# Kernel optimization log

Hardware: AMD Instinct MI355X
Metric: run time of the kernel (lower is better)

Reference implementation:

```python
import jax, jax.numpy as jnp
import numpy as np

# ---- Clifford algebra Cl(3,0) setup: blades ordered by grade ----
_BLADES = [(), (1,), (2,), (3,), (1, 2), (1, 3), (2, 3), (1, 2, 3)]
_SUBSPACES = np.array([1, 3, 3, 1])  # grade sizes
_GRADE_SLICES = [(0, 1), (1, 4), (4, 7), (7, 8)]


def _blade_mul(a, b):
    """Geometric product of two basis blades in Cl(3,0) (metric +1,+1,+1)."""
    arr = list(a) + list(b)
    sign = 1
    n = len(arr)
    for i in range(n):
        for j in range(n - 1):
            if arr[j] > arr[j + 1]:
                arr[j], arr[j + 1] = arr[j + 1], arr[j]
                sign = -sign
    res = []
    i = 0
    while i < len(arr):
        if i + 1 < len(arr) and arr[i] == arr[i + 1]:
            i += 2  # e_i * e_i = +1
        else:
            res.append(arr[i]); i += 1
    return sign, tuple(res)


def build_cayley():
    idx = {b: i for i, b in enumerate(_BLADES)}
    C = np.zeros((8, 8, 8), np.float32)
    for i, bi in enumerate(_BLADES):
        for k, bk in enumerate(_BLADES):
            s, r = _blade_mul(bi, bk)
            C[i, idx[r], k] = s
    return jnp.asarray(C)  # cayley[i, j, k]: coeff of blade j in (blade_i * blade_k)


def mv_linear(x, W):
    # x: (b, seq_in, 8); W: (seq_out, seq_in, 4) -> expand per-grade weight over blades
    Wfull = jnp.repeat(W, _SUBSPACES, axis=-1)  # (out, in, 8)
    return jnp.einsum('bmi,nmi->bni', x, Wfull)


def normalize(x, a):
    # x: (b, s, 8); a: (max_seq, 4)
    seq = x.shape[1]
    norms = jnp.concatenate(
        [jnp.linalg.norm(x[..., s:e], axis=-1, keepdims=True) for s, e in _GRADE_SLICES],
        axis=-1)  # (b, s, 4)
    s_a = jax.nn.sigmoid(a[:seq])                      # (s, 4)
    norms = s_a * (norms - 1.0) + 1.0                  # (b, s, 4)
    norms = jnp.repeat(norms, _SUBSPACES, axis=-1)     # (b, s, 8)
    return x / (norms + 1e-6)


def setup_inputs() -> dict:
    key = jax.random.key(0)
    k1, k2, k3 = jax.random.split(key, 3)
    B, S, D = 2, 2048, 8
    scale = 1.0 / np.sqrt(S)
    x = jax.random.normal(k1, (B, S, D), jnp.float32)
    Wq = jax.random.normal(k2, (S, S, 4), jnp.float32) * scale
    Wk = jax.random.normal(k3, (S, S, 4), jnp.float32) * scale
    a = jnp.zeros((3000, 4), jnp.float32)  # NormalizationLayer init=0
    return {"x": x, "Wq": Wq, "Wk": Wk, "a": a}


def reference(x, Wq, Wk, a):
    cayley = build_cayley()
    q = normalize(mv_linear(x, Wq), a)  # (b, s, 8)
    k = normalize(mv_linear(x, Wk), a)  # (b, s, 8)
    # pairwise geometric product: out[b,s,t,j] = sum_{i,k} q[b,s,i] cayley[i,j,k] k[b,t,k]
    tmp = jnp.einsum('bsi,ijk->bsjk', q, cayley)        # (b, s, 8, 8)
    out = jnp.einsum('bsjk,btk->bstj', tmp, k)          # (b, s, t, 8)
    return out
```

## Files before the change

### kernel.cpp

```cpp
#include <hip/hip_runtime.h>
#include <cmath>

#define SEQ 2048
#define BATCH 2

typedef float v4f __attribute__((ext_vector_type(4)));

__global__ __launch_bounds__(256) void qk_kernel(
    const float* __restrict__ x,
    const float* __restrict__ Wq,
    const float* __restrict__ Wk,
    const float* __restrict__ a,
    float* __restrict__ qout,
    float* __restrict__ kout)
{
    const int n   = blockIdx.x;
    const int tid = threadIdx.x;

    float acc[32];
#pragma unroll
    for (int v = 0; v < 32; v++) acc[v] = 0.f;

    const v4f* wq4 = (const v4f*)(Wq + (size_t)n * SEQ * 4);
    const v4f* wk4 = (const v4f*)(Wk + (size_t)n * SEQ * 4);
    const v4f* x4  = (const v4f*)x;

    for (int m = tid; m < SEQ; m += 256) {
        v4f wq = wq4[m];
        v4f wk = wk4[m];
        const float wqg[4] = {wq.x, wq.y, wq.z, wq.w};
        const float wkg[4] = {wk.x, wk.y, wk.z, wk.w};
#pragma unroll
        for (int b = 0; b < BATCH; b++) {
            v4f xa = x4[((size_t)b * SEQ + m) * 2];
            v4f xb = x4[((size_t)b * SEQ + m) * 2 + 1];
            const float xv[8] = {xa.x, xa.y, xa.z, xa.w, xb.x, xb.y, xb.z, xb.w};
            const int g[8] = {0, 1, 1, 1, 2, 2, 2, 3};
#pragma unroll
            for (int i = 0; i < 8; i++) {
                acc[0 * 16 + b * 8 + i] += wqg[g[i]] * xv[i];
                acc[1 * 16 + b * 8 + i] += wkg[g[i]] * xv[i];
            }
        }
    }

#pragma unroll
    for (int v = 0; v < 32; v++) {
#pragma unroll
        for (int off = 32; off >= 1; off >>= 1)
            acc[v] += __shfl_down(acc[v], off, 64);
    }

    __shared__ float red[4][32];
    __shared__ float fin[32];
    const int wave = tid >> 6;
    const int lane = tid & 63;
    if (lane == 0) {
#pragma unroll
        for (int v = 0; v < 32; v++) red[wave][v] = acc[v];
    }
    __syncthreads();
    if (tid < 32) fin[tid] = red[0][tid] + red[1][tid] + red[2][tid] + red[3][tid];
    __syncthreads();

    if (tid < 4) {
        const int t_sel = tid >> 1;
        const int b     = tid & 1;
        float v[8];
#pragma unroll
        for (int i = 0; i < 8; i++) v[i] = fin[t_sel * 16 + b * 8 + i];

        float nr[4];
        nr[0] = fabsf(v[0]);
        nr[1] = sqrtf(v[1] * v[1] + v[2] * v[2] + v[3] * v[3]);
        nr[2] = sqrtf(v[4] * v[4] + v[5] * v[5] + v[6] * v[6]);
        nr[3] = fabsf(v[7]);

        float sc[4];
#pragma unroll
        for (int gg = 0; gg < 4; gg++) {
            float sg = 1.f / (1.f + __expf(-a[n * 4 + gg]));
            sc[gg]   = 1.f / (sg * (nr[gg] - 1.f) + 1.f + 1e-6f);
        }

        float* dst = (t_sel ? kout : qout) + ((size_t)b * SEQ + n) * 8;
        const int g[8] = {0, 1, 1, 1, 2, 2, 2, 3};
#pragma unroll
        for (int i = 0; i < 8; i++) dst[i] = v[i] * sc[g[i]];
    }
}

__global__ __launch_bounds__(256) void gp_kernel(
    const float* __restrict__ q,
    const float* __restrict__ k,
    float* __restrict__ out)
{
    const int bs  = blockIdx.x;
    const int b   = bs >> 11;
    const int s   = bs & (SEQ - 1);
    const int tid = threadIdx.x;

    __shared__ float qs[8];
    if (tid < 8) qs[tid] = q[((size_t)b * SEQ + s) * 8 + tid];
    __syncthreads();
    const float q0 = qs[0], q1 = qs[1], q2 = qs[2], q3 = qs[3],
                q4 = qs[4], q5 = qs[5], q6 = qs[6], q7 = qs[7];

    const v4f* kp  = (const v4f*)(k + (size_t)b * SEQ * 8);
    v4f* out4 = (v4f*)(out + ((size_t)b * SEQ + s) * (size_t)SEQ * 8);

#pragma unroll
    for (int j = 0; j < 8; j++) {
        const int t = tid + j * 256;
        v4f ka = kp[t * 2];
        v4f kb = kp[t * 2 + 1];
        const float k0 = ka.x, k1 = ka.y, k2 = ka.z, k3 = ka.w;
        const float k4 = kb.x, k5 = kb.y, k6 = kb.z, k7 = kb.w;

        v4f oa, ob;
        oa.x = q0*k0 + q1*k1 + q2*k2 + q3*k3 - q4*k4 - q5*k5 - q6*k6 - q7*k7;
        oa.y = q0*k1 + q1*k0 - q2*k4 - q3*k5 + q4*k2 + q5*k3 - q6*k7 - q7*k6;
        oa.z = q0*k2 + q1*k4 + q2*k0 - q3*k6 - q4*k1 + q5*k7 + q6*k3 + q7*k5;
        oa.w = q0*k3 + q1*k5 + q2*k6 + q3*k0 - q4*k7 - q5*k1 - q6*k2 - q7*k4;
        ob.x = q0*k4 + q1*k2 - q2*k1 + q3*k7 + q4*k0 - q5*k6 + q6*k5 + q7*k3;
        ob.y = q0*k5 + q1*k3 - q2*k7 - q3*k1 + q4*k6 + q5*k0 - q6*k4 - q7*k2;
        ob.z = q0*k6 + q1*k7 + q2*k3 - q3*k2 - q4*k5 + q5*k4 + q6*k0 + q7*k1;
        ob.w = q0*k7 + q1*k6 - q2*k5 + q3*k4 + q4*k3 - q5*k2 + q6*k1 + q7*k0;

        __builtin_nontemporal_store(oa, &out4[t * 2]);
        __builtin_nontemporal_store(ob, &out4[t * 2 + 1]);
    }
}

extern "C" void kernel_launch(void* const* d_in, const int* in_sizes, int n_in,
                              void* d_out, int out_size, void* d_ws, size_t ws_size,
                              hipStream_t stream) {
    const float* x  = (const float*)d_in[0];
    const float* Wq = (const float*)d_in[1];
    const float* Wk = (const float*)d_in[2];
    const float* a  = (const float*)d_in[3];
    float* out = (float*)d_out;

    float* q = (float*)d_ws;
    float* k = q + (size_t)BATCH * SEQ * 8;

    qk_kernel<<<SEQ, 256, 0, stream>>>(x, Wq, Wk, a, q, k);
    gp_kernel<<<BATCH * SEQ, 256, 0, stream>>>(q, k, out);
}
```

Measured before the change: 464.7 us.

## Split Q/K projection across thread halves and make geometric-product stores contiguous

The projection kernel now gives Wq to one half of the block and Wk to the other, which halves per-thread accumulators. The shuffle-heavy reduction is replaced by a padded LDS transpose followed by a short 8-lane shuffle. The geometric-product kernel now has adjacent thread pairs each write one 16-byte half of an output element, so each wave's stores form one contiguous run instead of two strided ones. The cost is that each pair computes all eight outputs twice and loads k twice, doubling ALU and k-load work in the kernel that is bound by output writes.

```diff
diff --git a/kernel.cpp b/kernel.cpp
--- a/kernel.cpp
+++ b/kernel.cpp
@@ -14,22 +14,22 @@
     float* __restrict__ qout,
     float* __restrict__ kout)
 {
-    const int n   = blockIdx.x;
-    const int tid = threadIdx.x;
+    const int n     = blockIdx.x;
+    const int tid   = threadIdx.x;
+    const int t_sel = tid >> 7;
+    const int tl    = tid & 127;
 
-    float acc[32];
+    const float* W  = t_sel ? Wk : Wq;
+    const v4f* w4   = (const v4f*)(W + (size_t)n * SEQ * 4);
+    const v4f* x4   = (const v4f*)x;
+
+    float acc[16];
 #pragma unroll
-    for (int v = 0; v < 32; v++) acc[v] = 0.f;
+    for (int v = 0; v < 16; v++) acc[v] = 0.f;
 
-    const v4f* wq4 = (const v4f*)(Wq + (size_t)n * SEQ * 4);
-    const v4f* wk4 = (const v4f*)(Wk + (size_t)n * SEQ * 4);
-    const v4f* x4  = (const v4f*)x;
-
-    for (int m = tid; m < SEQ; m += 256) {
-        v4f wq = wq4[m];
-        v4f wk = wk4[m];
-        const float wqg[4] = {wq.x, wq.y, wq.z, wq.w};
-        const float wkg[4] = {wk.x, wk.y, wk.z, wk.w};
+    for (int m = tl; m < SEQ; m += 128) {
+        v4f w = w4[m];
+        const float wg[4] = {w.x, w.y, w.z, w.w};
 #pragma unroll
         for (int b = 0; b < BATCH; b++) {
             v4f xa = x4[((size_t)b * SEQ + m) * 2];
@@ -37,38 +37,38 @@
             const float xv[8] = {xa.x, xa.y, xa.z, xa.w, xb.x, xb.y, xb.z, xb.w};
             const int g[8] = {0, 1, 1, 1, 2, 2, 2, 3};
 #pragma unroll
-            for (int i = 0; i < 8; i++) {
-                acc[0 * 16 + b * 8 + i] += wqg[g[i]] * xv[i];
-                acc[1 * 16 + b * 8 + i] += wkg[g[i]] * xv[i];
-            }
+            for (int i = 0; i < 8; i++)
+                acc[b * 8 + i] += wg[g[i]] * xv[i];
         }
     }
 
+    __shared__ float lds[32 * 129];
+    __shared__ float fin[32];
 #pragma unroll
-    for (int v = 0; v < 32; v++) {
+    for (int v = 0; v < 16; v++)
+        lds[(t_sel * 16 + v) * 129 + tl] = acc[v];
+    __syncthreads();
+
+    {
+        const int v    = tid >> 3;
+        const int sgrp = tid & 7;
+        const float* row = &lds[v * 129 + sgrp * 16];
+        float p = 0.f;
 #pragma unroll
-        for (int off = 32; off >= 1; off >>= 1)
-            acc[v] += __shfl_down(acc[v], off, 64);
+        for (int i = 0; i < 16; i++) p += row[i];
+        p += __shfl_down(p, 4, 8);
+        p += __shfl_down(p, 2, 8);
+        p += __shfl_down(p, 1, 8);
+        if (sgrp == 0) fin[v] = p;
     }
-
-    __shared__ float red[4][32];
-    __shared__ float fin[32];
-    const int wave = tid >> 6;
-    const int lane = tid & 63;
-    if (lane == 0) {
-#pragma unroll
-        for (int v = 0; v < 32; v++) red[wave][v] = acc[v];
-    }
-    __syncthreads();
-    if (tid < 32) fin[tid] = red[0][tid] + red[1][tid] + red[2][tid] + red[3][tid];
     __syncthreads();
 
     if (tid < 4) {
-        const int t_sel = tid >> 1;
-        const int b     = tid & 1;
+        const int ts = tid >> 1;
+        const int b  = tid & 1;
         float v[8];
 #pragma unroll
-        for (int i = 0; i < 8; i++) v[i] = fin[t_sel * 16 + b * 8 + i];
+        for (int i = 0; i < 8; i++) v[i] = fin[ts * 16 + b * 8 + i];
 
         float nr[4];
         nr[0] = fabsf(v[0]);
@@ -83,7 +83,7 @@
             sc[gg]   = 1.f / (sg * (nr[gg] - 1.f) + 1.f + 1e-6f);
         }
 
-        float* dst = (t_sel ? kout : qout) + ((size_t)b * SEQ + n) * 8;
+        float* dst = (ts ? kout : qout) + ((size_t)b * SEQ + n) * 8;
         const int g[8] = {0, 1, 1, 1, 2, 2, 2, 3};
 #pragma unroll
         for (int i = 0; i < 8; i++) dst[i] = v[i] * sc[g[i]];
@@ -106,12 +106,15 @@
     const float q0 = qs[0], q1 = qs[1], q2 = qs[2], q3 = qs[3],
                 q4 = qs[4], q5 = qs[5], q6 = qs[6], q7 = qs[7];
 
-    const v4f* kp  = (const v4f*)(k + (size_t)b * SEQ * 8);
+    const v4f* kp = (const v4f*)(k + (size_t)b * SEQ * 8);
     v4f* out4 = (v4f*)(out + ((size_t)b * SEQ + s) * (size_t)SEQ * 8);
 
-#pragma unroll
-    for (int j = 0; j < 8; j++) {
-        const int t = tid + j * 256;
+    const bool hi = (tid & 1);
+
+#pragma unroll 4
+    for (int j = 0; j < 16; j++) {
+        const int f = tid + j * 256;
+        const int t = f >> 1;
         v4f ka = kp[t * 2];
         v4f kb = kp[t * 2 + 1];
         const float k0 = ka.x, k1 = ka.y, k2 = ka.z, k3 = ka.w;
@@ -127,8 +130,8 @@
         ob.z = q0*k6 + q1*k7 + q2*k3 - q3*k2 - q4*k5 + q5*k4 + q6*k0 + q7*k1;
         ob.w = q0*k7 + q1*k6 - q2*k5 + q3*k4 + q4*k3 - q5*k2 + q6*k1 + q7*k0;
 
-        __builtin_nontemporal_store(oa, &out4[t * 2]);
-        __builtin_nontemporal_store(ob, &out4[t * 2 + 1]);
+        v4f o = hi ? ob : oa;
+        __builtin_nontemporal_store(o, &out4[f]);
     }
 }
 
```

New measurement: 376.8 us. 18.9% less time.
